# Kernel tuning notes

Measured on AMD Instinct MI355X. Metric: run time of the kernel, lower is better.

Reference implementation:

```python
import jax, jax.numpy as jnp
import numpy as np
from jax import lax

C = 512   # n_feat == Cn == Cdim (forced by DA_conv/CA_layer consistency)
H, W = 16, 32  # reshape_codebooks(512)
K = 3     # kernel_size
RED = 8   # reduction


def _lrelu(x):
    return jax.nn.leaky_relu(x, 0.1)


def _conv1x1(x, w, b=None):
    # x: (B,C,H,W), w: (O,C) -- torch Conv2d(.,.,1) weight squeezed
    y = jnp.einsum('oc,bchw->bohw', w, x)
    if b is not None:
        y = y + b[None, :, None, None]
    return y


def _conv3x3(x, w, b):
    # x: (B,C,H,W), w: (O,C,3,3) OIHW, padding=k//2 == SAME for odd k
    y = lax.conv_general_dilated(x, w, (1, 1), 'SAME',
                                 dimension_numbers=('NCHW', 'OIHW', 'NCHW'))
    return y + b[None, :, None, None]


def _da_conv(c, deg, kw1, kw2, pw, pb, caw1, caw2):
    # per-channel dynamic kernels from degradation vectors: (Cn, K*K)
    kern = (_lrelu(deg @ kw1.T) @ kw2.T).reshape(C, 1, K, K)
    # depthwise conv, groups = b1*c1 = C (b1 == 1)
    out = lax.conv_general_dilated(c, kern, (1, 1), 'SAME',
                                   feature_group_count=C,
                                   dimension_numbers=('NCHW', 'OIHW', 'NCHW'))
    out = _lrelu(out)
    out = _conv1x1(out, pw, pb)
    # CA_layer: deg reshaped to (1, Cn, 16, 32), channel attention, deg * att
    dr = deg.reshape(1, C, H, W)
    att = jax.nn.sigmoid(_conv1x1(_lrelu(_conv1x1(dr, caw1)), caw2))
    return out + dr * att


def setup_inputs() -> dict:
    key = jax.random.key(0)
    ks = jax.random.split(key, 16)
    n = lambda i, shape, s=0.05: jax.random.normal(ks[i], shape, dtype=jnp.float32) * s
    return dict(
        c=jax.random.normal(ks[0], (1, C, H, W), dtype=jnp.float32),
        deg=jax.random.normal(ks[1], (C, C), dtype=jnp.float32) * 0.1,
        k1_w1=n(2, (C, C)), k1_w2=n(3, (K * K, C)),
        p1_w=n(4, (C, C)), p1_b=jnp.zeros((C,), jnp.float32),
        ca1_w1=n(5, (C // RED, C)), ca1_w2=n(6, (C, C // RED)),
        conv1_w=n(7, (C, C, K, K)), conv1_b=jnp.zeros((C,), jnp.float32),
        k2_w1=n(8, (C, C)), k2_w2=n(9, (K * K, C)),
        p2_w=n(10, (C, C)), p2_b=jnp.zeros((C,), jnp.float32),
        ca2_w1=n(11, (C // RED, C)), ca2_w2=n(12, (C, C // RED)),
        conv2_w=n(13, (C, C, K, K)), conv2_b=jnp.zeros((C,), jnp.float32),
    )


def reference(c, deg, k1_w1, k1_w2, p1_w, p1_b, ca1_w1, ca1_w2,
              conv1_w, conv1_b, k2_w1, k2_w2, p2_w, p2_b,
              ca2_w1, ca2_w2, conv2_w, conv2_b):
    out = _lrelu(_da_conv(c, deg, k1_w1, k1_w2, p1_w, p1_b, ca1_w1, ca1_w2))
    out = _lrelu(_conv3x3(out, conv1_w, conv1_b))
    out = _lrelu(_da_conv(out, deg, k2_w1, k2_w2, p2_w, p2_b, ca2_w1, ca2_w2))
    return _conv3x3(out, conv2_w, conv2_b) + c
```

## Files before the change

kernel.cpp:

```cpp
#include <hip/hip_runtime.h>
#include <hip/hip_bf16.h>

typedef __attribute__((ext_vector_type(8))) unsigned short ushort8;
typedef __attribute__((ext_vector_type(8))) __bf16 bf16x8;
typedef __attribute__((ext_vector_type(4))) float f32x4;
typedef __attribute__((ext_vector_type(4))) unsigned short ushort4v;

__device__ __forceinline__ float lrelu_f(float v){ return v > 0.f ? v : 0.1f*v; }

__device__ __forceinline__ unsigned short f2bf(float v){
  unsigned u = __float_as_uint(v);
  unsigned r = (u + 0x7fffu + ((u>>16)&1u)) >> 16;
  return (unsigned short)r;
}

__device__ __forceinline__ void packq(const float* __restrict__ s,
                                      unsigned short* __restrict__ d, int i){
  const float4 v = ((const float4*)s)[i];
  ushort4v o; o.x=f2bf(v.x); o.y=f2bf(v.y); o.z=f2bf(v.z); o.w=f2bf(v.w);
  *(ushort4v*)(d + (size_t)i*4) = o;
}

__global__ __launch_bounds__(256) void k_pack_all(
  const float* __restrict__ k1_w1, const float* __restrict__ k2_w1,
  const float* __restrict__ p1_w,  const float* __restrict__ p2_w,
  const float* __restrict__ ca1_w1,const float* __restrict__ ca1_w2,
  const float* __restrict__ ca2_w1,const float* __restrict__ ca2_w2,
  const float* __restrict__ deg,   const float* __restrict__ conv1_w,
  const float* __restrict__ conv2_w,
  unsigned short* __restrict__ K1B, unsigned short* __restrict__ K2B,
  unsigned short* __restrict__ P1B, unsigned short* __restrict__ P2B,
  unsigned short* __restrict__ CA1A,unsigned short* __restrict__ CA1B,
  unsigned short* __restrict__ CA2A,unsigned short* __restrict__ CA2B,
  unsigned short* __restrict__ DEGB,unsigned short* __restrict__ DEGT,
  unsigned short* __restrict__ WB1, unsigned short* __restrict__ WB2){
  int i = blockIdx.x*256 + threadIdx.x;
  if (i < 65536){ packq(k1_w1, K1B, i); return; } i -= 65536;
  if (i < 65536){ packq(k2_w1, K2B, i); return; } i -= 65536;
  if (i < 65536){ packq(p1_w,  P1B, i); return; } i -= 65536;
  if (i < 65536){ packq(p2_w,  P2B, i); return; } i -= 65536;
  if (i < 8192){ packq(ca1_w1, CA1A, i); return; } i -= 8192;
  if (i < 8192){ packq(ca1_w2, CA1B, i); return; } i -= 8192;
  if (i < 8192){ packq(ca2_w1, CA2A, i); return; } i -= 8192;
  if (i < 8192){ packq(ca2_w2, CA2B, i); return; } i -= 8192;
  if (i < 65536){ packq(deg, DEGB, i); return; } i -= 65536;
  if (i < 65536){
    const int j = i*4; const int p = j>>9, c = j&511;
    ushort4v o;
    o.x = f2bf(deg[(size_t)(c+0)*512 + p]);
    o.y = f2bf(deg[(size_t)(c+1)*512 + p]);
    o.z = f2bf(deg[(size_t)(c+2)*512 + p]);
    o.w = f2bf(deg[(size_t)(c+3)*512 + p]);
    *(ushort4v*)(DEGT + (size_t)j) = o;
    return;
  } i -= 65536;
  if (i < 589824){
    const int o_ = i/1152; const int r4 = (i - o_*1152)*4;
    const int t = r4>>9; const int ci = r4&511;
    const float* s = conv1_w + (size_t)o_*4608;
    ushort4v o;
    o.x = f2bf(s[(ci+0)*9 + t]); o.y = f2bf(s[(ci+1)*9 + t]);
    o.z = f2bf(s[(ci+2)*9 + t]); o.w = f2bf(s[(ci+3)*9 + t]);
    *(ushort4v*)(WB1 + (size_t)o_*4608 + r4) = o;
    return;
  } i -= 589824;
  if (i < 589824){
    const int o_ = i/1152; const int r4 = (i - o_*1152)*4;
    const int t = r4>>9; const int ci = r4&511;
    const float* s = conv2_w + (size_t)o_*4608;
    ushort4v o;
    o.x = f2bf(s[(ci+0)*9 + t]); o.y = f2bf(s[(ci+1)*9 + t]);
    o.z = f2bf(s[(ci+2)*9 + t]); o.w = f2bf(s[(ci+3)*9 + t]);
    *(ushort4v*)(WB2 + (size_t)o_*4608 + r4) = o;
  }
}

__device__ __forceinline__ void gemm64(
    const unsigned short* __restrict__ A, const unsigned short* __restrict__ Bt,
    int m0, int n0, int K, int tid,
    unsigned short* lA, unsigned short* lB, f32x4 acc[2][2]){
  const int wid = tid>>6, lane = tid&63;
  const int srow = tid>>2, skb = tid&3;
  const unsigned short* gA = A  + (size_t)(m0+srow)*K + skb*8;
  const unsigned short* gB = Bt + (size_t)(n0+srow)*K + skb*8;
  const int soff = srow*32 + 8*(skb ^ (srow&3));
  const int wr = (wid>>1)*32, wc = (wid&1)*32;
  const int l15 = lane&15, lkb = lane>>4;
  int aoff[2], boff[2];
  #pragma unroll
  for (int s=0;s<2;s++){
    const int Ra = wr + s*16 + l15;
    aoff[s] = Ra*32 + 8*(lkb ^ (Ra&3));
    const int Rb = wc + s*16 + l15;
    boff[s] = Rb*32 + 8*(lkb ^ (Rb&3));
  }
  const int nst = K>>5;
  ushort8 ra = *(const ushort8*)gA;
  ushort8 rb = *(const ushort8*)gB;
  *(ushort8*)(lA + soff) = ra;
  *(ushort8*)(lB + soff) = rb;
  if (nst > 1){ ra = *(const ushort8*)(gA+32); rb = *(const ushort8*)(gB+32); }
  __syncthreads();
  for (int st=0; st<nst; ++st){
    const int cur = (st&1)*2048;
    bf16x8 af[2], bfr[2];
    #pragma unroll
    for (int s=0;s<2;s++){
      af[s]  = *(const bf16x8*)(lA + cur + aoff[s]);
      bfr[s] = *(const bf16x8*)(lB + cur + boff[s]);
    }
    if (st+1 < nst){
      const int nxt = ((st+1)&1)*2048;
      *(ushort8*)(lA + nxt + soff) = ra;
      *(ushort8*)(lB + nxt + soff) = rb;
      if (st+2 < nst){
        ra = *(const ushort8*)(gA + (size_t)(st+2)*32);
        rb = *(const ushort8*)(gB + (size_t)(st+2)*32);
      }
    }
    #pragma unroll
    for (int mi=0;mi<2;mi++)
      #pragma unroll
      for (int ni=0;ni<2;ni++)
        acc[mi][ni] = __builtin_amdgcn_mfma_f32_16x16x32_bf16(af[mi], bfr[ni], acc[mi][ni], 0,0,0);
    __syncthreads();
  }
}

__global__ __launch_bounds__(256) void k_mgemm_pre(
    const unsigned short* __restrict__ DEGB, const unsigned short* __restrict__ DEGT,
    const unsigned short* __restrict__ K1B,  const unsigned short* __restrict__ K2B,
    const unsigned short* __restrict__ CA1A, const unsigned short* __restrict__ CA2A,
    float* __restrict__ TMP1, float* __restrict__ TMP2,
    unsigned short* __restrict__ HID1, unsigned short* __restrict__ HID2){
  const int z = blockIdx.z;
  if (z >= 2 && blockIdx.y != 0) return;
  const unsigned short* A  = (z < 2) ? DEGB : DEGT;
  const unsigned short* Bt = (z==0) ? K1B : (z==1) ? K2B : (z==2) ? CA1A : CA2A;
  __shared__ unsigned short lA[4096], lB[4096];
  const int tid = threadIdx.x;
  const int m0 = blockIdx.x*64, n0 = blockIdx.y*64;
  f32x4 acc[2][2] = {};
  gemm64(A, Bt, m0, n0, 512, tid, lA, lB, acc);

  const int wid = tid>>6, lane = tid&63;
  const int wr = (wid>>1)*32, wc = (wid&1)*32;
  const int l15 = lane&15, lkb = lane>>4;
  #pragma unroll
  for (int mi=0;mi<2;mi++)
    #pragma unroll
    for (int ni=0;ni<2;ni++){
      const int row = m0 + wr + mi*16 + lkb*4;
      const int col = n0 + wc + ni*16 + l15;
      #pragma unroll
      for (int r=0;r<4;r++){
        const float v = lrelu_f(acc[mi][ni][r]);
        if (z==0)      TMP1[(size_t)(row+r)*512 + col] = v;
        else if (z==1) TMP2[(size_t)(row+r)*512 + col] = v;
        else if (z==2) HID1[(size_t)(row+r)*64 + col] = f2bf(v);
        else           HID2[(size_t)(row+r)*64 + col] = f2bf(v);
      }
    }
}

__global__ __launch_bounds__(256) void k_kern_att(
    const float* __restrict__ TMP1, const float* __restrict__ TMP2,
    const float* __restrict__ kw2a, const float* __restrict__ kw2b,
    const unsigned short* __restrict__ CA1B, const unsigned short* __restrict__ CA2B,
    const unsigned short* __restrict__ HID1, const unsigned short* __restrict__ HID2,
    float* __restrict__ kern0, float* __restrict__ kern1,
    float* __restrict__ ATT1, float* __restrict__ ATT2){
  const int z = blockIdx.z;
  const int tid = threadIdx.x;
  if (z < 2){
    const float* tmp  = z ? TMP2 : TMP1;
    const float* kw2  = z ? kw2b : kw2a;
    float* kern       = z ? kern1 : kern0;
    const int i = blockIdx.x*4 + (tid>>6);
    const int lane = tid&63;
    float acc[9];
    #pragma unroll
    for (int q=0;q<9;q++) acc[q]=0.f;
    for (int j=lane; j<512; j+=64){
      const float t = tmp[i*512 + j];
      #pragma unroll
      for (int q=0;q<9;q++) acc[q] += t*kw2[q*512 + j];
    }
    #pragma unroll
    for (int q=0;q<9;q++){
      float v = acc[q];
      #pragma unroll
      for (int off=32; off>0; off>>=1) v += __shfl_down(v, off);
      if (lane==0) kern[i*9+q] = v;
    }
  } else {
    if (blockIdx.x >= 64) return;
    const unsigned short* A  = (z==2) ? CA1B : CA2B;
    const unsigned short* Bt = (z==2) ? HID1 : HID2;
    float* ATT               = (z==2) ? ATT1 : ATT2;
    __shared__ unsigned short lA[4096], lB[4096];
    const int m0 = (blockIdx.x>>3)*64, n0 = (blockIdx.x&7)*64;
    f32x4 acc[2][2] = {};
    gemm64(A, Bt, m0, n0, 64, tid, lA, lB, acc);
    const int wid = tid>>6, lane = tid&63;
    const int wr = (wid>>1)*32, wc = (wid&1)*32;
    const int l15 = lane&15, lkb = lane>>4;
    #pragma unroll
    for (int mi=0;mi<2;mi++)
      #pragma unroll
      for (int ni=0;ni<2;ni++){
        const int row = m0 + wr + mi*16 + lkb*4;
        const int col = n0 + wc + ni*16 + l15;
        #pragma unroll
        for (int r=0;r<4;r++)
          ATT[(size_t)(row+r)*512 + col] = 1.f/(1.f + expf(-acc[mi][ni][r]));
      }
  }
}

__global__ __launch_bounds__(512) void k_dwconv(const float* __restrict__ x,
    const float* __restrict__ kern, unsigned short* __restrict__ yt){
  const int c = blockIdx.x;
  const int p = threadIdx.x;
  const int iy = p>>5, ix = p&31;
  __shared__ float plane[18*34];
  for (int i=p;i<18*34;i+=512) plane[i]=0.f;
  __syncthreads();
  plane[(iy+1)*34 + ix+1] = x[c*512 + p];
  __syncthreads();
  const float* kp = kern + c*9;
  float s = 0.f;
  #pragma unroll
  for (int dy=0;dy<3;dy++)
    #pragma unroll
    for (int dx=0;dx<3;dx++)
      s += plane[(iy+dy)*34 + ix+dx]*kp[dy*3+dx];
  yt[(size_t)p*512 + c] = f2bf(lrelu_f(s));
}

__global__ __launch_bounds__(512) void k_dwconv_red(const float* __restrict__ part,
    const float* __restrict__ bias, const float* __restrict__ kern,
    unsigned short* __restrict__ yt, int nchunks){
  const int c = blockIdx.x;
  const int p = threadIdx.x;
  const int iy = p>>5, ix = p&31;
  __shared__ float plane[18*34];
  for (int i=p;i<18*34;i+=512) plane[i]=0.f;
  __syncthreads();
  if (p < 128){
    const float b = bias[c];
    float4 a4 = {b,b,b,b};
    for (int s=0;s<nchunks;s++){
      const float4 v = ((const float4*)(part + (size_t)s*262144 + c*512))[p];
      a4.x += v.x; a4.y += v.y; a4.z += v.z; a4.w += v.w;
    }
    a4.x = lrelu_f(a4.x); a4.y = lrelu_f(a4.y);
    a4.z = lrelu_f(a4.z); a4.w = lrelu_f(a4.w);
    const int px0 = p*4;
    float* dst = &plane[((px0>>5)+1)*34 + (px0&31)+1];
    dst[0]=a4.x; dst[1]=a4.y; dst[2]=a4.z; dst[3]=a4.w;
  }
  __syncthreads();
  const float* kp = kern + c*9;
  float s = 0.f;
  #pragma unroll
  for (int dy=0;dy<3;dy++)
    #pragma unroll
    for (int dx=0;dx<3;dx++)
      s += plane[(iy+dy)*34 + ix+dx]*kp[dy*3+dx];
  yt[(size_t)p*512 + c] = f2bf(lrelu_f(s));
}

__global__ __launch_bounds__(256) void k_pw(
    const unsigned short* __restrict__ A, const unsigned short* __restrict__ Bt,
    const float* __restrict__ bias,
    const float* __restrict__ E1, const float* __restrict__ E2,
    unsigned short* __restrict__ XT){
  __shared__ unsigned short lA[2][1024], lB[2][1024];
  __shared__ float tile[32][33];
  const int tid = threadIdx.x;
  const int wid = tid>>6, lane = tid&63;
  const int M0 = blockIdx.x*32, N0 = blockIdx.y*32;

  const int half = tid>>7;
  const int st_ = tid&127;
  const int srow = st_>>2, skb = st_&3;
  const unsigned short* gS = (half ? Bt + (size_t)(N0+srow)*512
                                   : A  + (size_t)(M0+srow)*512) + skb*8;
  unsigned short (*lS)[1024] = half ? lB : lA;
  const int soff = srow*32 + 8*(skb ^ (srow&3));

  const int wr = (wid>>1)*16, wc = (wid&1)*16;
  const int l15 = lane&15, lkb = lane>>4;
  const int Ra = wr + l15, Rb = wc + l15;
  const int aoff = Ra*32 + 8*(lkb ^ (Ra&3));
  const int boff = Rb*32 + 8*(lkb ^ (Rb&3));

  f32x4 acc = {};
  ushort8 r0 = *(const ushort8*)gS;
  *(ushort8*)(&lS[0][soff]) = r0;
  r0 = *(const ushort8*)(gS+32);
  __syncthreads();
  for (int st=0; st<16; ++st){
    const int cur = st&1;
    const bf16x8 af = *(const bf16x8*)(&lA[cur][aoff]);
    const bf16x8 bf = *(const bf16x8*)(&lB[cur][boff]);
    if (st+1 < 16){
      *(ushort8*)(&lS[cur^1][soff]) = r0;
      if (st+2 < 16) r0 = *(const ushort8*)(gS + (size_t)(st+2)*32);
    }
    acc = __builtin_amdgcn_mfma_f32_16x16x32_bf16(af, bf, acc, 0,0,0);
    __syncthreads();
  }

  #pragma unroll
  for (int r=0;r<4;r++){
    const int rl = wr + lkb*4 + r;
    const int cl = wc + l15;
    const int rr = M0 + rl, col = N0 + cl;
    float v = acc[r] + bias[rr] + E1[(size_t)rr*512+col]*E2[(size_t)rr*512+col];
    tile[rl][cl] = lrelu_f(v);
  }
  __syncthreads();
  const int pr = tid>>3, q = tid&7;
  ushort4v o;
  o.x = f2bf(tile[q*4+0][pr]); o.y = f2bf(tile[q*4+1][pr]);
  o.z = f2bf(tile[q*4+2][pr]); o.w = f2bf(tile[q*4+3][pr]);
  *(ushort4v*)(XT + (size_t)(N0+pr)*512 + M0 + q*4) = o;
}

template<int KCH>
__global__ __launch_bounds__(256) void k_mfma_conv(
    const unsigned short* __restrict__ WB,
    const unsigned short* __restrict__ XT,
    float* __restrict__ part){
  __shared__ unsigned short lA[2][2048], lB[2][4096];
  const int tid = threadIdx.x;
  const int wid = tid>>6, lane = tid&63;
  const int m0 = blockIdx.x*64, n0 = blockIdx.y*128;
  const int k0 = blockIdx.z*KCH;

  const int srow = tid>>2, skb = tid&3;
  const unsigned short* gA = WB + (size_t)(m0+srow)*4608 + k0 + skb*8;
  const int soffA = srow*32 + 8*(skb ^ (srow&3));
  const int brow1 = srow + 64;
  const int p0 = n0 + srow, p1 = n0 + brow1;
  const int py0 = p0>>5, px0 = p0&31, py1 = p1>>5, px1 = p1&31;
  const int soffB0 = srow*32 + 8*(skb ^ (srow&3));
  const int soffB1 = brow1*32 + 8*(skb ^ (brow1&3));

  const int wr = (wid>>1)*32, wc = (wid&1)*64;
  const int l15 = lane&15, lkb = lane>>4;
  int aoff[2], boff[4];
  #pragma unroll
  for (int s=0;s<2;s++){
    const int Ra = wr + s*16 + l15;
    aoff[s] = Ra*32 + 8*(lkb ^ (Ra&3));
  }
  #pragma unroll
  for (int u=0;u<4;u++){
    const int Rb = wc + u*16 + l15;
    boff[u] = Rb*32 + 8*(lkb ^ (Rb&3));
  }

  auto ldB = [&](int st, int py, int px)->ushort8 {
    const int k = k0 + st*32;
    const int t = k>>9;
    const int dy = t/3, dx = t - dy*3;
    const int yy = py + dy - 1, xx = px + dx - 1;
    ushort8 r = {};
    if ((unsigned)yy < 16u && (unsigned)xx < 32u)
      r = *(const ushort8*)(XT + (size_t)(yy*32+xx)*512 + (k&511) + skb*8);
    return r;
  };

  constexpr int NST = KCH/32;
  f32x4 acc[2][4] = {};
  ushort8 ra  = *(const ushort8*)gA;
  ushort8 rb0 = ldB(0, py0, px0);
  ushort8 rb1 = ldB(0, py1, px1);
  *(ushort8*)(&lA[0][soffA])  = ra;
  *(ushort8*)(&lB[0][soffB0]) = rb0;
  *(ushort8*)(&lB[0][soffB1]) = rb1;
  if (NST > 1){
    ra  = *(const ushort8*)(gA+32);
    rb0 = ldB(1, py0, px0);
    rb1 = ldB(1, py1, px1);
  }
  __syncthreads();
  for (int st=0; st<NST; ++st){
    const int cur = st&1;
    bf16x8 af[2], bfr[4];
    #pragma unroll
    for (int s=0;s<2;s++) af[s] = *(const bf16x8*)(&lA[cur][aoff[s]]);
    #pragma unroll
    for (int u=0;u<4;u++) bfr[u] = *(const bf16x8*)(&lB[cur][boff[u]]);
    if (st+1 < NST){
      const int nxt = cur^1;
      *(ushort8*)(&lA[nxt][soffA])  = ra;
      *(ushort8*)(&lB[nxt][soffB0]) = rb0;
      *(ushort8*)(&lB[nxt][soffB1]) = rb1;
      if (st+2 < NST){
        ra  = *(const ushort8*)(gA + (size_t)(st+2)*32);
        rb0 = ldB(st+2, py0, px0);
        rb1 = ldB(st+2, py1, px1);
      }
    }
    #pragma unroll
    for (int s=0;s<2;s++)
      #pragma unroll
      for (int u=0;u<4;u++)
        acc[s][u] = __builtin_amdgcn_mfma_f32_16x16x32_bf16(af[s], bfr[u], acc[s][u], 0,0,0);
    __syncthreads();
  }

  float* pbase = part + (size_t)blockIdx.z*262144;
  #pragma unroll
  for (int s=0;s<2;s++)
    #pragma unroll
    for (int u=0;u<4;u++){
      const int row = m0 + wr + s*16 + lkb*4;
      const int col = n0 + wc + u*16 + l15;
      #pragma unroll
      for (int r=0;r<4;r++)
        pbase[(size_t)(row+r)*512 + col] = acc[s][u][r];
    }
}

__global__ __launch_bounds__(256) void k_reduce_final(const float* __restrict__ part,
    const float* __restrict__ bias, const float* __restrict__ res,
    float* __restrict__ y, int nchunks){
  const int i = blockIdx.x*256 + threadIdx.x;
  const int o = i>>7;
  const float b = bias[o];
  float4 a4 = {b,b,b,b};
  for (int s=0;s<nchunks;s++){
    const float4 v = ((const float4*)part)[(size_t)s*65536 + i];
    a4.x += v.x; a4.y += v.y; a4.z += v.z; a4.w += v.w;
  }
  const float4 rv = ((const float4*)res)[i];
  a4.x += rv.x; a4.y += rv.y; a4.z += rv.z; a4.w += rv.w;
  ((float4*)y)[i] = a4;
}

extern "C" void kernel_launch(void* const* d_in, const int* in_sizes, int n_in,
                              void* d_out, int out_size, void* d_ws, size_t ws_size,
                              hipStream_t stream) {
  (void)in_sizes; (void)n_in; (void)out_size;
  const float* xin    = (const float*)d_in[0];
  const float* deg    = (const float*)d_in[1];
  const float* k1_w1  = (const float*)d_in[2];
  const float* k1_w2  = (const float*)d_in[3];
  const float* p1_w   = (const float*)d_in[4];
  const float* p1_b   = (const float*)d_in[5];
  const float* ca1_w1 = (const float*)d_in[6];
  const float* ca1_w2 = (const float*)d_in[7];
  const float* conv1_w= (const float*)d_in[8];
  const float* conv1_b= (const float*)d_in[9];
  const float* k2_w1  = (const float*)d_in[10];
  const float* k2_w2  = (const float*)d_in[11];
  const float* p2_w   = (const float*)d_in[12];
  const float* p2_b   = (const float*)d_in[13];
  const float* ca2_w1 = (const float*)d_in[14];
  const float* ca2_w2 = (const float*)d_in[15];
  const float* conv2_w= (const float*)d_in[16];
  const float* conv2_b= (const float*)d_in[17];
  float* out = (float*)d_out;

  const bool big = ws_size >= (size_t)8202000*4;
  const int NS = big ? 16 : 8;

  float* ws = (float*)d_ws;
  float* PART = ws;  ws += (size_t)NS*262144;
  float* TMP1 = PART;
  float* TMP2 = PART + 262144;
  unsigned short* HID1 = (unsigned short*)(PART + 524288);
  unsigned short* HID2 = HID1 + 32768;
  float* KERN1 = ws;  ws += 4608;
  float* KERN2 = ws;  ws += 4608;
  float* ATT1  = ws;  ws += 262144;
  float* ATT2  = ws;  ws += 262144;
  unsigned short* DEGB = (unsigned short*)ws; ws += 131072;
  unsigned short* DEGT = (unsigned short*)ws; ws += 131072;
  unsigned short* K1B  = (unsigned short*)ws; ws += 131072;
  unsigned short* K2B  = (unsigned short*)ws; ws += 131072;
  unsigned short* P1B  = (unsigned short*)ws; ws += 131072;
  unsigned short* P2B  = (unsigned short*)ws; ws += 131072;
  unsigned short* CA1A = (unsigned short*)ws; ws += 16384;
  unsigned short* CA1B = (unsigned short*)ws; ws += 16384;
  unsigned short* CA2A = (unsigned short*)ws; ws += 16384;
  unsigned short* CA2B = (unsigned short*)ws; ws += 16384;
  unsigned short* DWLT = (unsigned short*)ws; ws += 131072;
  unsigned short* XT   = (unsigned short*)ws; ws += 131072;
  unsigned short* WB1  = (unsigned short*)ws; ws += 1179648;
  unsigned short* WB2  = (unsigned short*)ws; ws += 1179648;

  k_pack_all<<<6272,256,0,stream>>>(k1_w1,k2_w1,p1_w,p2_w,
      ca1_w1,ca1_w2,ca2_w1,ca2_w2, deg, conv1_w, conv2_w,
      K1B,K2B,P1B,P2B, CA1A,CA1B,CA2A,CA2B, DEGB,DEGT, WB1,WB2);

  k_mgemm_pre<<<dim3(8,8,4),256,0,stream>>>(DEGB,DEGT, K1B,K2B, CA1A,CA2A,
      TMP1,TMP2, HID1,HID2);
  k_kern_att<<<dim3(128,1,4),256,0,stream>>>(TMP1,TMP2, k1_w2,k2_w2,
      CA1B,CA2B, HID1,HID2, KERN1,KERN2, ATT1,ATT2);

  k_dwconv<<<512,512,0,stream>>>(xin, KERN1, DWLT);
  k_pw<<<dim3(16,16),256,0,stream>>>(P1B, DWLT, p1_b, deg, ATT1, XT);
  if (big) k_mfma_conv<288><<<dim3(8,4,16),256,0,stream>>>(WB1, XT, PART);
  else     k_mfma_conv<576><<<dim3(8,4,8), 256,0,stream>>>(WB1, XT, PART);
  k_dwconv_red<<<512,512,0,stream>>>(PART, conv1_b, KERN2, DWLT, NS);
  k_pw<<<dim3(16,16),256,0,stream>>>(P2B, DWLT, p2_b, deg, ATT2, XT);
  if (big) k_mfma_conv<288><<<dim3(8,4,16),256,0,stream>>>(WB2, XT, PART);
  else     k_mfma_conv<576><<<dim3(8,4,8), 256,0,stream>>>(WB2, XT, PART);
  k_reduce_final<<<256,256,0,stream>>>(PART, conv2_b, xin, out, NS);
}
```

Baseline: 87.92 us.

## Store split-K conv partials as bf16 and use 64-wide K stages

The 3x3 conv MFMA kernel now loads 64 K-elements per pipeline stage, with a larger LDS tile and an 8-way XOR swizzle. This halves the number of barriers per block. Split-K partial sums are written as bf16 instead of fp32, which halves partial traffic in the conv epilogue and in both reduction kernels. The split count is fixed at 18 chunks of 256, which gives more blocks and always fits the workspace. Rounding each partial to bf16 before summing adds error to the conv outputs.

After: 85.13 us. -3.2%, faster.

```diff
diff --git a/kernel.cpp b/kernel.cpp
--- a/kernel.cpp
+++ b/kernel.cpp
@@ -12,6 +12,9 @@
   unsigned u = __float_as_uint(v);
   unsigned r = (u + 0x7fffu + ((u>>16)&1u)) >> 16;
   return (unsigned short)r;
+}
+__device__ __forceinline__ float bf2f(unsigned short u){
+  return __uint_as_float(((unsigned)u)<<16);
 }
 
 __device__ __forceinline__ void packq(const float* __restrict__ s,
@@ -238,7 +241,7 @@
   yt[(size_t)p*512 + c] = f2bf(lrelu_f(s));
 }
 
-__global__ __launch_bounds__(512) void k_dwconv_red(const float* __restrict__ part,
+__global__ __launch_bounds__(512) void k_dwconv_red(const unsigned short* __restrict__ part,
     const float* __restrict__ bias, const float* __restrict__ kern,
     unsigned short* __restrict__ yt, int nchunks){
   const int c = blockIdx.x;
@@ -251,8 +254,8 @@
     const float b = bias[c];
     float4 a4 = {b,b,b,b};
     for (int s=0;s<nchunks;s++){
-      const float4 v = ((const float4*)(part + (size_t)s*262144 + c*512))[p];
-      a4.x += v.x; a4.y += v.y; a4.z += v.z; a4.w += v.w;
+      const ushort4v v = ((const ushort4v*)(part + (size_t)s*262144 + c*512))[p];
+      a4.x += bf2f(v.x); a4.y += bf2f(v.y); a4.z += bf2f(v.z); a4.w += bf2f(v.w);
     }
     a4.x = lrelu_f(a4.x); a4.y = lrelu_f(a4.y);
     a4.z = lrelu_f(a4.z); a4.w = lrelu_f(a4.w);
@@ -333,8 +336,9 @@
 __global__ __launch_bounds__(256) void k_mfma_conv(
     const unsigned short* __restrict__ WB,
     const unsigned short* __restrict__ XT,
-    float* __restrict__ part){
-  __shared__ unsigned short lA[2][2048], lB[2][4096];
+    unsigned short* __restrict__ part){
+  __shared__ unsigned short lA[2][4096];
+  __shared__ unsigned short lB[2][8192];
   const int tid = threadIdx.x;
   const int wid = tid>>6, lane = tid&63;
   const int m0 = blockIdx.x*64, n0 = blockIdx.y*128;
@@ -342,79 +346,94 @@
 
   const int srow = tid>>2, skb = tid&3;
   const unsigned short* gA = WB + (size_t)(m0+srow)*4608 + k0 + skb*8;
-  const int soffA = srow*32 + 8*(skb ^ (srow&3));
   const int brow1 = srow + 64;
   const int p0 = n0 + srow, p1 = n0 + brow1;
   const int py0 = p0>>5, px0 = p0&31, py1 = p1>>5, px1 = p1&31;
-  const int soffB0 = srow*32 + 8*(skb ^ (srow&3));
-  const int soffB1 = brow1*32 + 8*(skb ^ (brow1&3));
+  const int s7 = srow&7;
+  const int soffA0 = srow*64 + 8*(skb ^ s7);
+  const int soffA1 = srow*64 + 8*((skb+4) ^ s7);
+  const int soffB00 = soffA0,            soffB01 = soffA1;
+  const int soffB10 = brow1*64 + 8*(skb ^ s7);
+  const int soffB11 = brow1*64 + 8*((skb+4) ^ s7);
 
   const int wr = (wid>>1)*32, wc = (wid&1)*64;
   const int l15 = lane&15, lkb = lane>>4;
-  int aoff[2], boff[4];
+  int aoff[2][2], boff[4][2];
   #pragma unroll
   for (int s=0;s<2;s++){
     const int Ra = wr + s*16 + l15;
-    aoff[s] = Ra*32 + 8*(lkb ^ (Ra&3));
+    #pragma unroll
+    for (int h=0;h<2;h++) aoff[s][h] = Ra*64 + 8*((lkb+4*h) ^ (Ra&7));
   }
   #pragma unroll
   for (int u=0;u<4;u++){
     const int Rb = wc + u*16 + l15;
-    boff[u] = Rb*32 + 8*(lkb ^ (Rb&3));
-  }
-
-  auto ldB = [&](int st, int py, int px)->ushort8 {
-    const int k = k0 + st*32;
+    #pragma unroll
+    for (int h=0;h<2;h++) boff[u][h] = Rb*64 + 8*((lkb+4*h) ^ (Rb&7));
+  }
+
+  auto ldB = [&](int st, int py, int px, ushort8& lo, ushort8& hi){
+    const int k = k0 + st*64;
     const int t = k>>9;
     const int dy = t/3, dx = t - dy*3;
     const int yy = py + dy - 1, xx = px + dx - 1;
-    ushort8 r = {};
-    if ((unsigned)yy < 16u && (unsigned)xx < 32u)
-      r = *(const ushort8*)(XT + (size_t)(yy*32+xx)*512 + (k&511) + skb*8);
-    return r;
+    lo = (ushort8){}; hi = (ushort8){};
+    if ((unsigned)yy < 16u && (unsigned)xx < 32u){
+      const unsigned short* b = XT + (size_t)(yy*32+xx)*512 + (k&511) + skb*8;
+      lo = *(const ushort8*)b; hi = *(const ushort8*)(b+32);
+    }
   };
 
-  constexpr int NST = KCH/32;
+  constexpr int NST = KCH/64;
   f32x4 acc[2][4] = {};
-  ushort8 ra  = *(const ushort8*)gA;
-  ushort8 rb0 = ldB(0, py0, px0);
-  ushort8 rb1 = ldB(0, py1, px1);
-  *(ushort8*)(&lA[0][soffA])  = ra;
-  *(ushort8*)(&lB[0][soffB0]) = rb0;
-  *(ushort8*)(&lB[0][soffB1]) = rb1;
+  ushort8 ra0 = *(const ushort8*)gA;
+  ushort8 ra1 = *(const ushort8*)(gA+32);
+  ushort8 b00,b01,b10,b11;
+  ldB(0, py0, px0, b00, b01);
+  ldB(0, py1, px1, b10, b11);
+  *(ushort8*)(&lA[0][soffA0]) = ra0;  *(ushort8*)(&lA[0][soffA1]) = ra1;
+  *(ushort8*)(&lB[0][soffB00]) = b00; *(ushort8*)(&lB[0][soffB01]) = b01;
+  *(ushort8*)(&lB[0][soffB10]) = b10; *(ushort8*)(&lB[0][soffB11]) = b11;
   if (NST > 1){
-    ra  = *(const ushort8*)(gA+32);
-    rb0 = ldB(1, py0, px0);
-    rb1 = ldB(1, py1, px1);
+    ra0 = *(const ushort8*)(gA+64); ra1 = *(const ushort8*)(gA+96);
+    ldB(1, py0, px0, b00, b01);
+    ldB(1, py1, px1, b10, b11);
   }
   __syncthreads();
   for (int st=0; st<NST; ++st){
     const int cur = st&1;
-    bf16x8 af[2], bfr[4];
-    #pragma unroll
-    for (int s=0;s<2;s++) af[s] = *(const bf16x8*)(&lA[cur][aoff[s]]);
-    #pragma unroll
-    for (int u=0;u<4;u++) bfr[u] = *(const bf16x8*)(&lB[cur][boff[u]]);
+    bf16x8 af[2][2], bfr[4][2];
+    #pragma unroll
+    for (int s=0;s<2;s++)
+      #pragma unroll
+      for (int h=0;h<2;h++) af[s][h] = *(const bf16x8*)(&lA[cur][aoff[s][h]]);
+    #pragma unroll
+    for (int u=0;u<4;u++)
+      #pragma unroll
+      for (int h=0;h<2;h++) bfr[u][h] = *(const bf16x8*)(&lB[cur][boff[u][h]]);
     if (st+1 < NST){
       const int nxt = cur^1;
-      *(ushort8*)(&lA[nxt][soffA])  = ra;
-      *(ushort8*)(&lB[nxt][soffB0]) = rb0;
-      *(ushort8*)(&lB[nxt][soffB1]) = rb1;
+      *(ushort8*)(&lA[nxt][soffA0]) = ra0;  *(ushort8*)(&lA[nxt][soffA1]) = ra1;
+      *(ushort8*)(&lB[nxt][soffB00]) = b00; *(ushort8*)(&lB[nxt][soffB01]) = b01;
+      *(ushort8*)(&lB[nxt][soffB10]) = b10; *(ushort8*)(&lB[nxt][soffB11]) = b11;
       if (st+2 < NST){
-        ra  = *(const ushort8*)(gA + (size_t)(st+2)*32);
-        rb0 = ldB(st+2, py0, px0);
-        rb1 = ldB(st+2, py1, px1);
+        ra0 = *(const ushort8*)(gA + (size_t)(st+2)*64);
+        ra1 = *(const ushort8*)(gA + (size_t)(st+2)*64 + 32);
+        ldB(st+2, py0, px0, b00, b01);
+        ldB(st+2, py1, px1, b10, b11);
       }
     }
     #pragma unroll
-    for (int s=0;s<2;s++)
-      #pragma unroll
-      for (int u=0;u<4;u++)
-        acc[s][u] = __builtin_amdgcn_mfma_f32_16x16x32_bf16(af[s], bfr[u], acc[s][u], 0,0,0);
+    for (int h=0;h<2;h++)
+      #pragma unroll
+      for (int s=0;s<2;s++)
+        #pragma unroll
+        for (int u=0;u<4;u++)
+          acc[s][u] = __builtin_amdgcn_mfma_f32_16x16x32_bf16(af[s][h], bfr[u][h], acc[s][u], 0,0,0);
     __syncthreads();
   }
 
-  float* pbase = part + (size_t)blockIdx.z*262144;
+  unsigned short* pbase = part + (size_t)blockIdx.z*262144;
   #pragma unroll
   for (int s=0;s<2;s++)
     #pragma unroll
@@ -423,11 +442,11 @@
       const int col = n0 + wc + u*16 + l15;
       #pragma unroll
       for (int r=0;r<4;r++)
-        pbase[(size_t)(row+r)*512 + col] = acc[s][u][r];
-    }
-}
-
-__global__ __launch_bounds__(256) void k_reduce_final(const float* __restrict__ part,
+        pbase[(size_t)(row+r)*512 + col] = f2bf(acc[s][u][r]);
+    }
+}
+
+__global__ __launch_bounds__(256) void k_reduce_final(const unsigned short* __restrict__ part,
     const float* __restrict__ bias, const float* __restrict__ res,
     float* __restrict__ y, int nchunks){
   const int i = blockIdx.x*256 + threadIdx.x;
@@ -435,8 +454,8 @@
   const float b = bias[o];
   float4 a4 = {b,b,b,b};
   for (int s=0;s<nchunks;s++){
-    const float4 v = ((const float4*)part)[(size_t)s*65536 + i];
-    a4.x += v.x; a4.y += v.y; a4.z += v.z; a4.w += v.w;
+    const ushort4v v = ((const ushort4v*)part)[(size_t)s*65536 + i];
+    a4.x += bf2f(v.x); a4.y += bf2f(v.y); a4.z += bf2f(v.z); a4.w += bf2f(v.w);
   }
   const float4 rv = ((const float4*)res)[i];
   a4.x += rv.x; a4.y += rv.y; a4.z += rv.z; a4.w += rv.w;
@@ -446,7 +465,7 @@
 extern "C" void kernel_launch(void* const* d_in, const int* in_sizes, int n_in,
                               void* d_out, int out_size, void* d_ws, size_t ws_size,
                               hipStream_t stream) {
-  (void)in_sizes; (void)n_in; (void)out_size;
+  (void)in_sizes; (void)n_in; (void)out_size; (void)ws_size;
   const float* xin    = (const float*)d_in[0];
   const float* deg    = (const float*)d_in[1];
   const float* k1_w1  = (const float*)d_in[2];
@@ -467,14 +486,14 @@
   const float* conv2_b= (const float*)d_in[17];
   float* out = (float*)d_out;
 
-  const bool big = ws_size >= (size_t)8202000*4;
-  const int NS = big ? 16 : 8;
+  const int NS = 18;
 
   float* ws = (float*)d_ws;
-  float* PART = ws;  ws += (size_t)NS*262144;
-  float* TMP1 = PART;
-  float* TMP2 = PART + 262144;
-  unsigned short* HID1 = (unsigned short*)(PART + 524288);
+  unsigned short* PART = (unsigned short*)ws;
+  ws += (size_t)NS*131072;
+  float* TMP1 = (float*)PART;
+  float* TMP2 = TMP1 + 262144;
+  unsigned short* HID1 = (unsigned short*)(TMP2 + 262144);
   unsigned short* HID2 = HID1 + 32768;
   float* KERN1 = ws;  ws += 4608;
   float* KERN2 = ws;  ws += 4608;
@@ -506,11 +525,9 @@
 
   k_dwconv<<<512,512,0,stream>>>(xin, KERN1, DWLT);
   k_pw<<<dim3(16,16),256,0,stream>>>(P1B, DWLT, p1_b, deg, ATT1, XT);
-  if (big) k_mfma_conv<288><<<dim3(8,4,16),256,0,stream>>>(WB1, XT, PART);
-  else     k_mfma_conv<576><<<dim3(8,4,8), 256,0,stream>>>(WB1, XT, PART);
+  k_mfma_conv<256><<<dim3(8,4,18),256,0,stream>>>(WB1, XT, PART);
   k_dwconv_red<<<512,512,0,stream>>>(PART, conv1_b, KERN2, DWLT, NS);
   k_pw<<<dim3(16,16),256,0,stream>>>(P2B, DWLT, p2_b, deg, ATT2, XT);
-  if (big) k_mfma_conv<288><<<dim3(8,4,16),256,0,stream>>>(WB2, XT, PART);
-  else     k_mfma_conv<576><<<dim3(8,4,8), 256,0,stream>>>(WB2, XT, PART);
+  k_mfma_conv<256><<<dim3(8,4,18),256,0,stream>>>(WB2, XT, PART);
   k_reduce_final<<<256,256,0,stream>>>(PART, conv2_b, xin, out, NS);
 }
```
